# Kernel tuning notes

Hardware: AMD Instinct MI355X
Metric: run time of the kernel (lower is better)

Reference implementation:

```python
import jax, jax.numpy as jnp
import numpy as np

N, E, H, NH, S, EF, K = 25000, 400000, 64, 4, 16, 8, 2
HS = H // NH  # head size


def _ln(x, w, b):
    m = x.mean(-1, keepdims=True)
    v = ((x - m) ** 2).mean(-1, keepdims=True)
    return (x - m) / jnp.sqrt(v + 1e-5) * w + b


def _seg_softmax(scores, seg, n):
    # scores: [E, NH], seg: [E] -> softmax over edges sharing the same dest node
    mx = jax.ops.segment_max(scores, seg, num_segments=n)
    e = jnp.exp(scores - mx[seg])
    s = jax.ops.segment_sum(e, seg, num_segments=n)
    return e / (s[seg] + 1e-9)


def _edge_layer(h, x_s, src, dest, ef, w1, w2, proj, gated):
    # h: [N,H] (already layer-normed). Gather, fused per-edge MLP (no bias).
    inp = jnp.concatenate([h[src], h[dest], x_s[src], x_s[dest], ef], axis=-1)  # [E,168]
    raw = jnp.maximum(inp @ w1.T, 0.0) @ w2.T  # [E,NH]
    if gated:
        w = jax.nn.sigmoid(raw)
    else:
        w = _seg_softmax(jax.nn.leaky_relu(raw) / jnp.sqrt(jnp.asarray(HS, raw.dtype)), dest, N)
    msg = h.reshape(N, NH, HS)[src] * w[:, :, None]          # [E,NH,HS]
    agg = jax.ops.segment_sum(msg, dest, num_segments=N)     # [N,NH,HS]
    return agg.reshape(N, H) @ proj.T, w


def _mlp(x, w1, b1, w2, b2):
    return jnp.maximum(x @ w1.T + b1, 0.0) @ w2.T + b2


def _forward(x, x_s, edge_features, fwd_w1, fwd_w2, fwd_proj, rev_w1, rev_w2, rev_proj,
             ln_w, ln_b, r_w1, r_b1, r_w2, r_b2, z_w1, z_b1, z_w2, z_b2,
             c_w1, c_b1, c_w2, c_b2, edge_index):
    src, dest = edge_index[0], edge_index[1]
    # forward-direction stacked attention hops
    h_fwd, fwd_ws = x, []
    for k in range(K):
        h_norm = _ln(h_fwd, ln_w, ln_b)
        msg, w = _edge_layer(h_norm, x_s, src, dest, edge_features,
                             fwd_w1[k], fwd_w2[k], fwd_proj[k], gated=False)
        h_fwd = h_fwd + msg
        fwd_ws.append(w)
    fwd_ws = jnp.stack(fwd_ws, axis=-1)  # [E,NH,K]
    # reverse-direction stacked gating hops (edge direction flipped)
    h_rev, rev_ws = x, []
    for k in range(K):
        h_norm = _ln(h_rev, ln_w, ln_b)
        msg, w = _edge_layer(h_norm, x_s, dest, src, edge_features,
                             rev_w1[k], rev_w2[k], rev_proj[k], gated=True)
        h_rev = h_rev + msg
        rev_ws.append(w)
    rev_ws = jnp.stack(rev_ws, axis=-1)  # [E,NH,K]
    messages = jnp.concatenate([h_fwd - x, h_rev - x], axis=-1)  # [N,2H]
    gate_input = jnp.concatenate([x, messages], axis=-1)          # [N,3H]
    r_gate = jax.nn.sigmoid(_mlp(gate_input, r_w1, r_b1, r_w2, r_b2))
    z_gate = jax.nn.sigmoid(_mlp(gate_input, z_w1, z_b1, z_w2, z_b2))
    cand_in = jnp.concatenate([r_gate * x, messages], axis=-1)
    cand = jnp.tanh(_mlp(cand_in, c_w1, c_b1, c_w2, c_b2))
    final_h = (1.0 - z_gate) * x + z_gate * cand
    return final_h, fwd_ws, rev_ws, z_gate, r_gate


def setup_inputs() -> dict:
    key = jax.random.key(0)
    ks = jax.random.split(key, 20)
    mlp_in = 2 * H + 2 * S + EF  # 168
    width = 2 * H                # 128
    gi, gw = 3 * H, 3 * H        # 192, 192

    def nrm(k, shape, fan_in):
        return jax.random.normal(k, shape, jnp.float32) / np.sqrt(fan_in)

    return {
        'x': jax.random.normal(ks[0], (N, H), jnp.float32),
        'x_s': jax.random.normal(ks[1], (N, S), jnp.float32),
        'edge_index': jax.random.randint(ks[2], (2, E), 0, N, jnp.int32),
        'edge_features': jax.random.normal(ks[3], (E, EF), jnp.float32),
        'fwd_w1': nrm(ks[4], (K, width, mlp_in), mlp_in),
        'fwd_w2': nrm(ks[5], (K, NH, width), width),
        'fwd_proj': nrm(ks[6], (K, H, H), H),
        'rev_w1': nrm(ks[7], (K, width, mlp_in), mlp_in),
        'rev_w2': nrm(ks[8], (K, NH, width), width),
        'rev_proj': nrm(ks[9], (K, H, H), H),
        'ln_w': jnp.ones((H,), jnp.float32),
        'ln_b': jnp.zeros((H,), jnp.float32),
        'r_w1': nrm(ks[10], (gw, gi), gi), 'r_b1': jnp.zeros((gw,), jnp.float32),
        'r_w2': nrm(ks[11], (H, gw), gw), 'r_b2': jnp.zeros((H,), jnp.float32),
        'z_w1': nrm(ks[12], (gw, gi), gi), 'z_b1': jnp.zeros((gw,), jnp.float32),
        'z_w2': nrm(ks[13], (H, gw), gw), 'z_b2': jnp.zeros((H,), jnp.float32),
        'c_w1': nrm(ks[14], (gw, gi), gi), 'c_b1': jnp.zeros((gw,), jnp.float32),
        'c_w2': nrm(ks[15], (H, gw), gw), 'c_b2': jnp.zeros((H,), jnp.float32),
    }


def reference(x, x_s, edge_index, edge_features, fwd_w1, fwd_w2, fwd_proj,
              rev_w1, rev_w2, rev_proj, ln_w, ln_b, r_w1, r_b1, r_w2, r_b2,
              z_w1, z_b1, z_w2, z_b2, c_w1, c_b1, c_w2, c_b2):
    return _forward(x, x_s, edge_features, fwd_w1, fwd_w2, fwd_proj,
                    rev_w1, rev_w2, rev_proj, ln_w, ln_b,
                    r_w1, r_b1, r_w2, r_b2, z_w1, z_b1, z_w2, z_b2,
                    c_w1, c_b1, c_w2, c_b2, edge_index)
```

## Files before the change

kernel.cpp:

```cpp
#include <hip/hip_runtime.h>
#include <hip/hip_fp16.h>
#include <math.h>

#define NN 25000
#define EE 400000
#define HH 64
#define NHEAD 4
#define SDIM 16
#define EFDIM 8
#define KHOP 2
#define MIN 168
#define WID 128
#define GIN 192
#define KP 96

typedef __attribute__((ext_vector_type(8))) short bf16x8;
typedef __attribute__((ext_vector_type(4))) float f32x4;
typedef unsigned short ushortT;
typedef unsigned int uintT;

__device__ __forceinline__ float wave_sum64(float v) {
#pragma unroll
  for (int m = 1; m <= 32; m <<= 1) v += __shfl_xor(v, m, 64);
  return v;
}

__device__ __forceinline__ ushortT f2b(float f) {
  uintT u = __float_as_uint(f);
  return (ushortT)((u + 0x7FFFu + ((u >> 16) & 1u)) >> 16);
}
__device__ __forceinline__ float b2f(ushortT h) {
  return __uint_as_float(((uintT)h) << 16);
}

union U4H8 {
  uint4 u;
  __half2 h[4];
};

__device__ __forceinline__ __half2 relu2(__half2 v) {
  union { __half2 h; uintT u; } x;
  x.h = v;
  uintT mask = ((x.u & 0x80008000u) >> 15) * 0xFFFFu;
  x.u &= ~mask;
  return x.h;
}

__global__ void k_histo2(const int* __restrict__ src, const int* __restrict__ dst,
                         int* __restrict__ cnt_s, int* __restrict__ cnt_d) {
  int e = blockIdx.x * 256 + threadIdx.x;
  if (e < EE) {
    atomicAdd(&cnt_d[dst[e]], 1);
    atomicAdd(&cnt_s[src[e]], 1);
  }
}

__global__ void k_scan2(const int* __restrict__ cnt_d, const int* __restrict__ cnt_s,
                        int* __restrict__ rp_d, int* __restrict__ rp_s) {
  const int* cnt = blockIdx.x ? cnt_s : cnt_d;
  int* rp = blockIdx.x ? rp_s : rp_d;
  __shared__ int part[1024];
  int t = threadIdx.x;
  const int CH = (NN + 1023) / 1024;
  int base = t * CH;
  int s = 0;
  for (int i = 0; i < CH; ++i) {
    int j = base + i;
    if (j < NN) s += cnt[j];
  }
  part[t] = s;
  __syncthreads();
  for (int off = 1; off < 1024; off <<= 1) {
    int v = (t >= off) ? part[t - off] : 0;
    __syncthreads();
    part[t] += v;
    __syncthreads();
  }
  int run = (t == 0) ? 0 : part[t - 1];
  for (int i = 0; i < CH; ++i) {
    int j = base + i;
    if (j < NN) { rp[j] = run; run += cnt[j]; }
  }
  if (t == 1023) rp[NN] = run;
}

__global__ void k_scatter2(const int* __restrict__ src, const int* __restrict__ dst,
                           const int* __restrict__ rp_s, const int* __restrict__ rp_d,
                           int* __restrict__ cur_s, int* __restrict__ cur_d,
                           int* __restrict__ eid_s, int* __restrict__ eid_d) {
  int e = blockIdx.x * 256 + threadIdx.x;
  if (e < EE) {
    int nd = dst[e];
    int pd = atomicAdd(&cur_d[nd], 1);
    eid_d[rp_d[nd] + pd] = e;
    int ns = src[e];
    int ps = atomicAdd(&cur_s[ns], 1);
    eid_s[rp_s[ns] + ps] = e;
  }
}

__global__ __launch_bounds__(256) void k_sortseg2(const int* __restrict__ rp_d,
                                                  const int* __restrict__ rp_s,
                                                  int* __restrict__ eid_d,
                                                  int* __restrict__ eid_s) {
  int gw = blockIdx.x * 4 + (threadIdx.x >> 6);
  int lane = threadIdx.x & 63;
  if (gw >= 2 * NN) return;
  const int* rp = (gw < NN) ? rp_d : rp_s;
  int* eids = (gw < NN) ? eid_d : eid_s;
  int node = (gw < NN) ? gw : gw - NN;
  int beg = rp[node], end = rp[node + 1];
  int deg = end - beg;
  if (deg <= 1) return;
  if (deg <= 64) {
    int v = (lane < deg) ? eids[beg + lane] : 0x7fffffff;
#pragma unroll
    for (int k = 2; k <= 64; k <<= 1) {
#pragma unroll
      for (int j = k >> 1; j > 0; j >>= 1) {
        int other = __shfl_xor(v, j, 64);
        bool takeMin = (((lane & k) == 0) == ((lane & j) == 0));
        v = takeMin ? min(v, other) : max(v, other);
      }
    }
    if (lane < deg) eids[beg + lane] = v;
  } else if (lane == 0) {
    for (int i = beg + 1; i < end; ++i) {
      int v = eids[i];
      int j = i - 1;
      while (j >= beg && eids[j] > v) { eids[j + 1] = eids[j]; --j; }
      eids[j + 1] = v;
    }
  }
}

__global__ void k_mkpos2(const int* __restrict__ eid_d, const int* __restrict__ eid_s,
                         const int* __restrict__ src, const int* __restrict__ dst,
                         const float* __restrict__ ef, int4* __restrict__ pos_f,
                         int4* __restrict__ pos_r, uint4* __restrict__ efh_f,
                         uint4* __restrict__ efh_r) {
  int i = blockIdx.x * 256 + threadIdx.x;
  if (i >= EE) return;
  int e1 = eid_d[i];
  pos_f[i] = make_int4(e1, src[e1], dst[e1], 0);
  int e2 = eid_s[i];
  pos_r[i] = make_int4(e2, dst[e2], src[e2], 0);
  {
    float4 a0 = *(const float4*)(ef + (size_t)e1 * EFDIM);
    float4 a1 = *(const float4*)(ef + (size_t)e1 * EFDIM + 4);
    U4H8 u;
    u.h[0] = __floats2half2_rn(a0.x, a0.y);
    u.h[1] = __floats2half2_rn(a0.z, a0.w);
    u.h[2] = __floats2half2_rn(a1.x, a1.y);
    u.h[3] = __floats2half2_rn(a1.z, a1.w);
    efh_f[i] = u.u;
  }
  {
    float4 b0 = *(const float4*)(ef + (size_t)e2 * EFDIM);
    float4 b1 = *(const float4*)(ef + (size_t)e2 * EFDIM + 4);
    U4H8 u;
    u.h[0] = __floats2half2_rn(b0.x, b0.y);
    u.h[1] = __floats2half2_rn(b0.z, b0.w);
    u.h[2] = __floats2half2_rn(b1.x, b1.y);
    u.h[3] = __floats2half2_rn(b1.z, b1.w);
    efh_r[i] = u.u;
  }
}

#define PACKN (256 * KP + 512 + 256)
__global__ void k_pack_bf(const float* __restrict__ fw1, const float* __restrict__ rw1,
                          const float* __restrict__ fw2, const float* __restrict__ rw2,
                          ushortT* __restrict__ pAB_all, __half2* __restrict__ w1e2_all,
                          __half2* __restrict__ w22_all) {
  int y = blockIdx.y;
  const float* w1 = (y < 2) ? fw1 + (size_t)y * WID * MIN
                            : rw1 + (size_t)(y - 2) * WID * MIN;
  const float* w2 = (y < 2) ? fw2 + (size_t)y * NHEAD * WID
                            : rw2 + (size_t)(y - 2) * NHEAD * WID;
  int i = blockIdx.x * 256 + threadIdx.x;
  if (i < 256 * KP) {
    int j = i / KP, k = i % KP;
    float v = 0.f;
    if (k < 80) {
      int row = (j < 128) ? j : j - 128;
      int col = (j < 128) ? (k < 64 ? k : k + 64) : (k < 64 ? k + 64 : k + 80);
      v = w1[row * MIN + col];
    }
    pAB_all[(size_t)y * 256 * KP + i] = f2b(v);
  } else if (i < 256 * KP + 512) {
    int jj = i - 256 * KP;
    int f = jj >> 6, jp = jj & 63;
    w1e2_all[y * 512 + jj] =
        __floats2half2_rn(w1[(2 * jp) * MIN + 160 + f], w1[(2 * jp + 1) * MIN + 160 + f]);
  } else if (i < PACKN) {
    int jj = i - 256 * KP - 512;
    int o = jj >> 6, jp = jj & 63;
    w22_all[y * 256 + jj] = __floats2half2_rn(w2[o * WID + 2 * jp], w2[o * WID + 2 * jp + 1]);
  }
}

#define CW1 (GIN * GIN)
#define CW2 (HH * GIN)
__global__ void k_cvt6(const float* __restrict__ r_w1, const float* __restrict__ z_w1,
                       const float* __restrict__ c_w1, const float* __restrict__ r_w2,
                       const float* __restrict__ z_w2, const float* __restrict__ c_w2,
                       ushortT* __restrict__ rzw1, ushortT* __restrict__ cw1,
                       ushortT* __restrict__ rw2, ushortT* __restrict__ zw2,
                       ushortT* __restrict__ cw2) {
  int i = blockIdx.x * 256 + threadIdx.x;
  if (i < CW1) rzw1[i] = f2b(r_w1[i]);
  else if (i < 2 * CW1) rzw1[i] = f2b(z_w1[i - CW1]);
  else if (i < 3 * CW1) cw1[i - 2 * CW1] = f2b(c_w1[i - 2 * CW1]);
  else if (i < 3 * CW1 + CW2) rw2[i - 3 * CW1] = f2b(r_w2[i - 3 * CW1]);
  else if (i < 3 * CW1 + 2 * CW2) zw2[i - 3 * CW1 - CW2] = f2b(z_w2[i - 3 * CW1 - CW2]);
  else if (i < 3 * CW1 + 3 * CW2) cw2[i - 3 * CW1 - 2 * CW2] = f2b(c_w2[i - 3 * CW1 - 2 * CW2]);
}

__global__ __launch_bounds__(256) void k_ln_init(
    const float* __restrict__ x, const float* __restrict__ xs,
    const float* __restrict__ lw, const float* __restrict__ lb,
    ushortT* __restrict__ ncf0, ushortT* __restrict__ ncr0,
    ushortT* __restrict__ ncf1, ushortT* __restrict__ ncr1) {
  int t = threadIdx.x;
  int node = blockIdx.x * 4 + (t >> 6), lane = t & 63;
  if (node >= NN) return;
  float v = x[(size_t)node * HH + lane];
  float mean = wave_sum64(v) * (1.0f / 64.0f);
  float d = v - mean;
  float var = wave_sum64(d * d) * (1.0f / 64.0f);
  ushortT val = f2b(d * rsqrtf(var + 1e-5f) * lw[lane] + lb[lane]);
  ncf0[(size_t)node * KP + lane] = val;
  ncr0[(size_t)node * KP + lane] = val;
  if (lane < SDIM) {
    ushortT xv = f2b(xs[(size_t)node * SDIM + lane]);
    ncf0[(size_t)node * KP + HH + lane] = xv;
    ncr0[(size_t)node * KP + HH + lane] = xv;
    ncf1[(size_t)node * KP + HH + lane] = xv;
    ncr1[(size_t)node * KP + HH + lane] = xv;
    ncf0[(size_t)node * KP + 80 + lane] = 0;
    ncr0[(size_t)node * KP + 80 + lane] = 0;
    ncf1[(size_t)node * KP + 80 + lane] = 0;
    ncr1[(size_t)node * KP + 80 + lane] = 0;
  }
}

__global__ __launch_bounds__(256) void k_proj2(
    const ushortT* __restrict__ Af, const ushortT* __restrict__ Ar,
    const ushortT* __restrict__ Wf, const ushortT* __restrict__ Wr,
    ushortT* __restrict__ Cf, ushortT* __restrict__ Cr) {
  const ushortT* A = blockIdx.y ? Ar : Af;
  const ushortT* W = blockIdx.y ? Wr : Wf;
  ushortT* C = blockIdx.y ? Cr : Cf;
  int w = threadIdx.x >> 6, l = threadIdx.x & 63;
  int m0 = blockIdx.x * 64 + w * 16;
  int rowa = m0 + (l & 15);
  int kb = l >> 4;
  bf16x8 afr0 = {0,0,0,0,0,0,0,0}, afr1 = afr0, afr2 = afr0;
  if (rowa < NN) {
    const ushortT* ap = A + (size_t)rowa * KP + kb * 8;
    afr0 = *(const bf16x8*)(ap);
    afr1 = *(const bf16x8*)(ap + 32);
    afr2 = *(const bf16x8*)(ap + 64);
  }
  int crow = m0 + (l >> 4) * 4;
  int ccol0 = l & 15;
  for (int n0 = 0; n0 < 256; n0 += 64) {
    f32x4 acc[4];
#pragma unroll
    for (int n = 0; n < 4; ++n) acc[n] = (f32x4){0.f, 0.f, 0.f, 0.f};
    const ushortT* wbase = W + (size_t)(n0 + (l & 15)) * KP + kb * 8;
#pragma unroll
    for (int n = 0; n < 4; ++n) {
      const ushortT* wp = wbase + (size_t)(16 * n) * KP;
      acc[n] = __builtin_amdgcn_mfma_f32_16x16x32_bf16(afr0, *(const bf16x8*)(wp), acc[n], 0, 0, 0);
      acc[n] = __builtin_amdgcn_mfma_f32_16x16x32_bf16(afr1, *(const bf16x8*)(wp + 32), acc[n], 0, 0, 0);
      acc[n] = __builtin_amdgcn_mfma_f32_16x16x32_bf16(afr2, *(const bf16x8*)(wp + 64), acc[n], 0, 0, 0);
    }
#pragma unroll
    for (int n = 0; n < 4; ++n) {
      int col = n0 + ccol0 + n * 16;
#pragma unroll
      for (int r = 0; r < 4; ++r) {
        int row = crow + r;
        if (row < NN)
          C[(size_t)row * 256 + col] = __half_as_ushort(__float2half(acc[n][r]));
      }
    }
  }
}

template <int ACT, int BF16OUT, int KD>
__global__ __launch_bounds__(256) void k_gemm2(
    const ushortT* __restrict__ A, int lda, const ushortT* __restrict__ W,
    const float* __restrict__ bias, void* __restrict__ Cout, int ldc, int M, int Nc,
    const float* __restrict__ zv, const float* __restrict__ xp) {
  constexpr int KS = KD / 32;
  int w = threadIdx.x >> 6, l = threadIdx.x & 63;
  int m0 = blockIdx.x * 64 + w * 16;
  int rowa = m0 + (l & 15);
  int kb = l >> 4;
  bf16x8 afr[KS];
#pragma unroll
  for (int ks = 0; ks < KS; ++ks) {
    afr[ks] = (bf16x8){0, 0, 0, 0, 0, 0, 0, 0};
    if (rowa < M) afr[ks] = *(const bf16x8*)(A + (size_t)rowa * lda + ks * 32 + kb * 8);
  }
  int crow = m0 + (l >> 4) * 4;
  int ccol0 = l & 15;
  for (int n0 = 0; n0 < Nc; n0 += 64) {
    f32x4 acc[4];
#pragma unroll
    for (int n = 0; n < 4; ++n) acc[n] = (f32x4){0.f, 0.f, 0.f, 0.f};
    const ushortT* wbase = W + (size_t)(n0 + (l & 15)) * KD + kb * 8;
#pragma unroll
    for (int n = 0; n < 4; ++n) {
      const ushortT* wp = wbase + (size_t)(16 * n) * KD;
#pragma unroll
      for (int ks = 0; ks < KS; ++ks)
        acc[n] = __builtin_amdgcn_mfma_f32_16x16x32_bf16(afr[ks], *(const bf16x8*)(wp + ks * 32),
                                                         acc[n], 0, 0, 0);
    }
#pragma unroll
    for (int n = 0; n < 4; ++n) {
      int col = n0 + ccol0 + n * 16;
      float bv = bias ? bias[col] : 0.f;
#pragma unroll
      for (int r = 0; r < 4; ++r) {
        int row = crow + r;
        if (row < M) {
          float v = acc[n][r] + bv;
          if (ACT == 1) v = fmaxf(v, 0.f);
          else if (ACT == 2) v = 1.f / (1.f + expf(-v));
          else if (ACT == 3) v = tanhf(v);
          else if (ACT == 5) {
            float z = zv[(size_t)row * HH + col];
            float xv = xp[(size_t)row * HH + col];
            v = (1.f - z) * xv + z * tanhf(v);
          }
          if (BF16OUT)
            ((ushortT*)Cout)[(size_t)row * ldc + col] = f2b(v);
          else
            ((float*)Cout)[(size_t)row * ldc + col] = v;
        }
      }
    }
  }
}

__global__ __launch_bounds__(256) void k_gemm_rz(
    const ushortT* __restrict__ hid, const ushortT* __restrict__ rw2,
    const ushortT* __restrict__ zw2, const float* __restrict__ rb2,
    const float* __restrict__ zb2, float* __restrict__ outR, float* __restrict__ outZ,
    const float* __restrict__ x, ushortT* __restrict__ gi) {
  int y = blockIdx.y;
  const ushortT* A = hid + (y ? GIN : 0);
  const ushortT* W = y ? zw2 : rw2;
  const float* bias = y ? zb2 : rb2;
  float* C = y ? outZ : outR;
  constexpr int KS = GIN / 32;
  int w = threadIdx.x >> 6, l = threadIdx.x & 63;
  int m0 = blockIdx.x * 64 + w * 16;
  int rowa = m0 + (l & 15);
  int kb = l >> 4;
  bf16x8 afr[KS];
#pragma unroll
  for (int ks = 0; ks < KS; ++ks) {
    afr[ks] = (bf16x8){0, 0, 0, 0, 0, 0, 0, 0};
    if (rowa < NN) afr[ks] = *(const bf16x8*)(A + (size_t)rowa * 384 + ks * 32 + kb * 8);
  }
  int crow = m0 + (l >> 4) * 4;
  int ccol0 = l & 15;
  f32x4 acc[4];
#pragma unroll
  for (int n = 0; n < 4; ++n) acc[n] = (f32x4){0.f, 0.f, 0.f, 0.f};
  const ushortT* wbase = W + (size_t)(l & 15) * GIN + kb * 8;
#pragma unroll
  for (int n = 0; n < 4; ++n) {
    const ushortT* wp = wbase + (size_t)(16 * n) * GIN;
#pragma unroll
    for (int ks = 0; ks < KS; ++ks)
      acc[n] = __builtin_amdgcn_mfma_f32_16x16x32_bf16(afr[ks], *(const bf16x8*)(wp + ks * 32),
                                                       acc[n], 0, 0, 0);
  }
#pragma unroll
  for (int n = 0; n < 4; ++n) {
    int col = ccol0 + n * 16;
    float bv = bias[col];
#pragma unroll
    for (int r = 0; r < 4; ++r) {
      int row = crow + r;
      if (row < NN) {
        float v = acc[n][r] + bv;
        float sig = 1.f / (1.f + expf(-v));
        C[(size_t)row * HH + col] = sig;
        if (y == 0)
          gi[(size_t)row * GIN + col] = f2b(sig * x[(size_t)row * HH + col]);
      }
    }
  }
}

__global__ __launch_bounds__(256) void k_edge3(
    const ushortT* __restrict__ cABf, const ushortT* __restrict__ cABr,
    const int4* __restrict__ pos_f, const int4* __restrict__ pos_r,
    const uint4* __restrict__ efh_f, const uint4* __restrict__ efh_r,
    const __half2* __restrict__ w1e2_f, const __half2* __restrict__ w1e2_r,
    const __half2* __restrict__ w22_f, const __half2* __restrict__ w22_r,
    float* __restrict__ s_seq, float* __restrict__ outRW,
    float* __restrict__ ws_seq, int hop) {
  int y = blockIdx.y;
  const __half2* cAB2 = (const __half2*)(y ? cABr : cABf);
  const int4* pos = y ? pos_r : pos_f;
  const uint4* efh = y ? efh_r : efh_f;
  const __half2* w1e2 = y ? w1e2_r : w1e2_f;
  const __half2* w22 = y ? w22_r : w22_f;
  __shared__ __half2 w1e2_s[8][64];
  __shared__ __half2 w22_s[4][64];
  int t = threadIdx.x;
  for (int i = t; i < 512; i += 256) w1e2_s[i >> 6][i & 63] = w1e2[i];
  if (t < 256) w22_s[t >> 6][t & 63] = w22[t];
  __syncthreads();
  int es = t >> 2, q = t & 3;
  size_t ii = (size_t)blockIdx.x * 64 + es;
  int4 pr = pos[ii];
  const __half2* cA2 = cAB2 + (size_t)pr.y * 128;
  const __half2* cB2 = cAB2 + (size_t)pr.z * 128 + 64;
  U4H8 efu;
  efu.u = efh[ii];
  __half2 efb[8];
#pragma unroll
  for (int f2v = 0; f2v < 4; ++f2v) {
    efb[2 * f2v] = __half2half2(__low2half(efu.h[f2v]));
    efb[2 * f2v + 1] = __half2half2(__high2half(efu.h[f2v]));
  }
  float pf[4] = {0.f, 0.f, 0.f, 0.f};
#pragma unroll
  for (int c = 0; c < 4; ++c) {
    int jp0 = c * 16 + q * 4;
    U4H8 ua, ub;
    ua.u = *(const uint4*)(cA2 + jp0);
    ub.u = *(const uint4*)(cB2 + jp0);
    __half2 h2v[4];
#pragma unroll
    for (int i2 = 0; i2 < 4; ++i2) h2v[i2] = __hadd2(ua.h[i2], ub.h[i2]);
#pragma unroll
    for (int f = 0; f < 8; ++f) {
      U4H8 wv;
      wv.u = *(const uint4*)(&w1e2_s[f][jp0]);
#pragma unroll
      for (int i2 = 0; i2 < 4; ++i2) h2v[i2] = __hfma2(efb[f], wv.h[i2], h2v[i2]);
    }
#pragma unroll
    for (int i2 = 0; i2 < 4; ++i2) h2v[i2] = relu2(h2v[i2]);
#pragma unroll
    for (int o = 0; o < 4; ++o) {
      U4H8 wv;
      wv.u = *(const uint4*)(&w22_s[o][jp0]);
      __half2 p2 = __hmul2(h2v[0], wv.h[0]);
      p2 = __hfma2(h2v[1], wv.h[1], p2);
      p2 = __hfma2(h2v[2], wv.h[2], p2);
      p2 = __hfma2(h2v[3], wv.h[3], p2);
      pf[o] += __low2float(p2) + __high2float(p2);
    }
  }
#pragma unroll
  for (int m = 1; m <= 2; m <<= 1) {
    pf[0] += __shfl_xor(pf[0], m, 64);
    pf[1] += __shfl_xor(pf[1], m, 64);
    pf[2] += __shfl_xor(pf[2], m, 64);
    pf[3] += __shfl_xor(pf[3], m, 64);
  }
  float pv = (q == 0) ? pf[0] : (q == 1) ? pf[1] : (q == 2) ? pf[2] : pf[3];
  if (y) {
    float sig = 1.f / (1.f + expf(-pv));
    outRW[(size_t)pr.x * (NHEAD * KHOP) + q * KHOP + hop] = sig;
    ws_seq[ii * 4 + q] = sig;
  } else {
    s_seq[ii * 4 + q] = (pv > 0.f ? pv : 0.01f * pv) * 0.25f;
  }
}

template <int DO_LN, int DO_GATE>
__global__ __launch_bounds__(256) void k_softagg4(
    const ushortT* __restrict__ ncf, const ushortT* __restrict__ ncr,
    ushortT* __restrict__ ncf_n, ushortT* __restrict__ ncr_n,
    const float* __restrict__ s_seq, const float* __restrict__ ws_seq, int hop,
    const int* __restrict__ rp_d, const int* __restrict__ rp_s,
    const int4* __restrict__ pos_f, const int4* __restrict__ pos_r,
    const float* __restrict__ proj_f, const float* __restrict__ proj_r,
    float* __restrict__ h_f, float* __restrict__ h_r, float* __restrict__ wout,
    const float* __restrict__ lnw, const float* __restrict__ lnb,
    const float* __restrict__ x, ushortT* __restrict__ gi) {
  int y = blockIdx.y;
  const ushortT* hn_bf = y ? ncr : ncf;
  const int* rp = y ? rp_s : rp_d;
  const int4* pos = y ? pos_r : pos_f;
  const float* proj = y ? proj_r : proj_f;
  float* h = y ? h_r : h_f;
  __shared__ float proj_s[64][68];
  __shared__ float agg_s[4][64];
  __shared__ float w_s[4][64][4];
  __shared__ int ot_s[4][64];
  int t = threadIdx.x;
  for (int i = t; i < 4096; i += 256) proj_s[i >> 6][i & 63] = proj[i];
  int wvi = t >> 6, lane = t & 63;
  __syncthreads();

  for (int it = 0; it < 4; ++it) {
    int node = blockIdx.x * 16 + wvi * 4 + it;
    if (node >= NN) continue;
    int beg = rp[node], end = rp[node + 1];
    int deg = end - beg;
    bool small = (deg <= 64);
    float mxv = 0.f, invv = 0.f;
    int li = lane >> 2, o = lane & 3;
    if (deg > 0 && small) {
      int i0 = beg + li;
      if (y == 0) {
        int ee4[4];
        float sv[4];
#pragma unroll
        for (int u = 0; u < 4; ++u) {
          int idx = i0 + u * 16;
          bool val = idx < end;
          int4 pr = pos[val ? idx : beg];
          ee4[u] = pr.x;
          if (o == 0 && val) ot_s[wvi][li + u * 16] = pr.y * KP;
          float v = s_seq[(size_t)(val ? idx : beg) * 4 + o];
          sv[u] = val ? v : -1e30f;
        }
        float mx = fmaxf(fmaxf(sv[0], sv[1]), fmaxf(sv[2], sv[3]));
#pragma unroll
        for (int m = 4; m <= 32; m <<= 1) mx = fmaxf(mx, __shfl_xor(mx, m, 64));
        float ex[4];
        float sum = 0.f;
#pragma unroll
        for (int u = 0; u < 4; ++u) {
          ex[u] = (sv[u] > -1e29f) ? expf(sv[u] - mx) : 0.f;
          sum += ex[u];
        }
#pragma unroll
        for (int m = 4; m <= 32; m <<= 1) sum += __shfl_xor(sum, m, 64);
        float inv = 1.f / (sum + 1e-9f);
#pragma unroll
        for (int u = 0; u < 4; ++u) {
          if (i0 + u * 16 < end) {
            float wv = ex[u] * inv;
            wout[(size_t)ee4[u] * (NHEAD * KHOP) + o * KHOP + hop] = wv;
            w_s[wvi][li + u * 16][o] = wv;
          }
        }
      } else {
#pragma unroll
        for (int u = 0; u < 4; ++u) {
          int idx = i0 + u * 16;
          bool val = idx < end;
          if (val) {
            if (o == 0) {
              int4 pr = pos[idx];
              ot_s[wvi][li + u * 16] = pr.y * KP;
            }
            w_s[wvi][li + u * 16][o] = ws_seq[(size_t)idx * 4 + o];
          }
        }
      }
    } else if (deg > 0) {
      if (y == 0) {
        float mx = -1e30f;
        for (int ii = beg + li; ii < end; ii += 16)
          mx = fmaxf(mx, s_seq[(size_t)ii * 4 + o]);
#pragma unroll
        for (int m = 4; m <= 32; m <<= 1) mx = fmaxf(mx, __shfl_xor(mx, m, 64));
        float sum = 0.f;
        for (int ii = beg + li; ii < end; ii += 16)
          sum += expf(s_seq[(size_t)ii * 4 + o] - mx);
#pragma unroll
        for (int m = 4; m <= 32; m <<= 1) sum += __shfl_xor(sum, m, 64);
        float inv = 1.f / (sum + 1e-9f);
        for (int ii = beg + li; ii < end; ii += 16) {
          wout[(size_t)pos[ii].x * (NHEAD * KHOP) + o * KHOP + hop] =
              expf(s_seq[(size_t)ii * 4 + o] - mx) * inv;
        }
        mxv = mx;
        invv = inv;
      }
    }
    int hd = lane >> 4;
    float acc = 0.f;
    if (small) {
      for (int ii = 0; ii < deg; ii += 8) {
#pragma unroll
        for (int u = 0; u < 8; ++u) {
          int ed = ii + u;
          int edc = (ed < deg) ? ed : 0;
          int ot = ot_s[wvi][edc];
          float w = w_s[wvi][edc][hd];
          float hv = b2f(hn_bf[(size_t)ot + lane]);
          acc += ((ed < deg) ? w : 0.f) * hv;
        }
      }
    } else {
      float mx_hd = 0.f, inv_hd = 0.f;
      if (y == 0) {
        mx_hd = __shfl(mxv, hd, 64);
        inv_hd = __shfl(invv, hd, 64);
      }
      for (int ii = beg; ii < end; ++ii) {
        int4 pr = pos[ii];
        float w;
        if (y == 0)
          w = expf(s_seq[(size_t)ii * 4 + hd] - mx_hd) * inv_hd;
        else
          w = ws_seq[(size_t)ii * 4 + hd];
        acc += w * b2f(hn_bf[(size_t)pr.y * KP + lane]);
      }
    }
    agg_s[wvi][lane] = acc;
    float m = 0.f;
#pragma unroll
    for (int hh = 0; hh < 64; hh += 4) {
      float4 p = *(const float4*)(&proj_s[lane][hh]);
      m += p.x * agg_s[wvi][hh] + p.y * agg_s[wvi][hh + 1] +
           p.z * agg_s[wvi][hh + 2] + p.w * agg_s[wvi][hh + 3];
    }
    size_t g = (size_t)node * HH + lane;
    float hnew = h[g] + m;
    h[g] = hnew;
    if (DO_LN) {
      float mean = wave_sum64(hnew) * (1.0f / 64.0f);
      float d = hnew - mean;
      float var = wave_sum64(d * d) * (1.0f / 64.0f);
      ushortT val = f2b(d * rsqrtf(var + 1e-5f) * lnw[lane] + lnb[lane]);
      (y ? ncr_n : ncf_n)[(size_t)node * KP + lane] = val;
    }
    if (DO_GATE) {
      float xv = x[g];
      if (y == 0) {
        gi[(size_t)node * GIN + lane] = f2b(xv);
        gi[(size_t)node * GIN + 64 + lane] = f2b(hnew - xv);
      } else {
        gi[(size_t)node * GIN + 128 + lane] = f2b(hnew - xv);
      }
    }
  }
}

extern "C" void kernel_launch(void* const* d_in, const int* in_sizes, int n_in,
                              void* d_out, int out_size, void* d_ws, size_t ws_size,
                              hipStream_t stream) {
  const float* x = (const float*)d_in[0];
  const float* xs = (const float*)d_in[1];
  const int* ei = (const int*)d_in[2];
  const float* ef = (const float*)d_in[3];
  const float* fw1 = (const float*)d_in[4];
  const float* fw2 = (const float*)d_in[5];
  const float* fpj = (const float*)d_in[6];
  const float* rw1 = (const float*)d_in[7];
  const float* rw2 = (const float*)d_in[8];
  const float* rpj = (const float*)d_in[9];
  const float* lnw = (const float*)d_in[10];
  const float* lnb = (const float*)d_in[11];
  const float* r_w1 = (const float*)d_in[12];
  const float* r_b1 = (const float*)d_in[13];
  const float* r_w2 = (const float*)d_in[14];
  const float* r_b2 = (const float*)d_in[15];
  const float* z_w1 = (const float*)d_in[16];
  const float* z_b1 = (const float*)d_in[17];
  const float* z_w2 = (const float*)d_in[18];
  const float* z_b2 = (const float*)d_in[19];
  const float* c_w1 = (const float*)d_in[20];
  const float* c_b1 = (const float*)d_in[21];
  const float* c_w2 = (const float*)d_in[22];
  const float* c_b2 = (const float*)d_in[23];
  const int* srcp = ei;
  const int* dstp = ei + EE;

  float* outF = (float*)d_out;
  float* outFW = outF + (size_t)NN * HH;
  float* outRW = outFW + (size_t)EE * NHEAD * KHOP;
  float* outZ = outRW + (size_t)EE * NHEAD * KHOP;
  float* outR = outZ + (size_t)NN * HH;

  char* Wb = (char*)d_ws;
  size_t off = 0;
  auto alloc = [&](size_t bytes) -> void* {
    void* p = Wb + off;
    off += (bytes + 255) & ~(size_t)255;
    return p;
  };
  float* h_fwd = (float*)alloc((size_t)NN * HH * 4);
  float* h_rev = (float*)alloc((size_t)NN * HH * 4);
  ushortT* ncat_f0 = (ushortT*)alloc((size_t)NN * KP * 2);
  ushortT* ncat_r0 = (ushortT*)alloc((size_t)NN * KP * 2);
  ushortT* ncat_f1 = (ushortT*)alloc((size_t)NN * KP * 2);
  ushortT* ncat_r1 = (ushortT*)alloc((size_t)NN * KP * 2);
  float* s_seq = (float*)alloc((size_t)EE * NHEAD * 4);
  float* ws_seq = (float*)alloc((size_t)EE * NHEAD * 4);
  char* big = (char*)alloc((size_t)2 * NN * 256 * 2);
  ushortT* cAB_f = (ushortT*)big;
  ushortT* cAB_r = (ushortT*)(big + (size_t)NN * 256 * 2);
  ushortT* hid_bf = (ushortT*)big;
  ushortT* gi_bf = (ushortT*)alloc((size_t)NN * GIN * 2);
  ushortT* packAB_bf = (ushortT*)alloc((size_t)4 * 256 * KP * 2);
  __half2* w1e2h = (__half2*)alloc((size_t)4 * 512 * 4);
  __half2* w22h = (__half2*)alloc((size_t)4 * 256 * 4);
  ushortT* rzw1_bf = (ushortT*)alloc((size_t)384 * GIN * 2);
  ushortT* rw2_bf = (ushortT*)alloc((size_t)HH * GIN * 2);
  ushortT* zw2_bf = (ushortT*)alloc((size_t)HH * GIN * 2);
  ushortT* cw1_bf = (ushortT*)alloc((size_t)GIN * GIN * 2);
  ushortT* cw2_bf = (ushortT*)alloc((size_t)HH * GIN * 2);
  float* rz_b1 = (float*)alloc(384 * 4);
  int* rp_d = (int*)alloc((NN + 8) * 4);
  int* rp_s = (int*)alloc((NN + 8) * 4);
  int* cur2 = (int*)alloc((size_t)2 * NN * 4);
  int* cur_d = cur2;
  int* cur_s = cur2 + NN;
  int* eid_d = (int*)alloc((size_t)EE * 4);
  int* eid_s = (int*)alloc((size_t)EE * 4);
  int4* pos_f = (int4*)alloc((size_t)EE * 16);
  int4* pos_r = (int4*)alloc((size_t)EE * 16);
  uint4* efh_f = (uint4*)alloc((size_t)EE * 16);
  uint4* efh_r = (uint4*)alloc((size_t)EE * 16);

  (void)hipMemcpyAsync(h_fwd, x, (size_t)NN * HH * 4, hipMemcpyDeviceToDevice, stream);
  (void)hipMemcpyAsync(h_rev, x, (size_t)NN * HH * 4, hipMemcpyDeviceToDevice, stream);
  (void)hipMemcpyAsync(rz_b1, r_b1, GIN * 4, hipMemcpyDeviceToDevice, stream);
  (void)hipMemcpyAsync(rz_b1 + GIN, z_b1, GIN * 4, hipMemcpyDeviceToDevice, stream);

  const int EB = (EE + 255) / 256, NW = (NN + 3) / 4;
  const int PB = (PACKN + 255) / 256;

  dim3 gPack(PB, 4);
  k_pack_bf<<<gPack, 256, 0, stream>>>(fw1, rw1, fw2, rw2, packAB_bf, w1e2h, w22h);
  k_cvt6<<<(3 * CW1 + 3 * CW2 + 255) / 256, 256, 0, stream>>>(
      r_w1, z_w1, c_w1, r_w2, z_w2, c_w2, rzw1_bf, cw1_bf, rw2_bf, zw2_bf, cw2_bf);

  (void)hipMemsetAsync(cur2, 0, (size_t)2 * NN * 4, stream);
  k_histo2<<<EB, 256, 0, stream>>>(srcp, dstp, cur_s, cur_d);
  k_scan2<<<2, 1024, 0, stream>>>(cur_d, cur_s, rp_d, rp_s);
  (void)hipMemsetAsync(cur2, 0, (size_t)2 * NN * 4, stream);
  k_scatter2<<<EB, 256, 0, stream>>>(srcp, dstp, rp_s, rp_d, cur_s, cur_d, eid_s, eid_d);
  k_sortseg2<<<(2 * NN + 3) / 4, 256, 0, stream>>>(rp_d, rp_s, eid_d, eid_s);
  k_mkpos2<<<EB, 256, 0, stream>>>(eid_d, eid_s, srcp, dstp, ef, pos_f, pos_r, efh_f, efh_r);

  k_ln_init<<<NW, 256, 0, stream>>>(x, xs, lnw, lnb, ncat_f0, ncat_r0, ncat_f1, ncat_r1);

  const int MB64 = (NN + 63) / 64;
  const int NB16 = (NN + 15) / 16;
  dim3 gProj(MB64, 2), gEdge(EE / 64, 2), gAgg(NB16, 2);
  for (int k = 0; k < KHOP; ++k) {
    const ushortT* nf = k ? ncat_f1 : ncat_f0;
    const ushortT* nr = k ? ncat_r1 : ncat_r0;
    k_proj2<<<gProj, 256, 0, stream>>>(nf, nr,
                                       packAB_bf + (size_t)k * 256 * KP,
                                       packAB_bf + (size_t)(2 + k) * 256 * KP,
                                       cAB_f, cAB_r);
    k_edge3<<<gEdge, 256, 0, stream>>>(cAB_f, cAB_r, pos_f, pos_r, efh_f, efh_r,
                                       w1e2h + (size_t)k * 512,
                                       w1e2h + (size_t)(2 + k) * 512,
                                       w22h + (size_t)k * 256,
                                       w22h + (size_t)(2 + k) * 256,
                                       s_seq, outRW, ws_seq, k);
    if (k == 0)
      k_softagg4<1, 0><<<gAgg, 256, 0, stream>>>(
          nf, nr, ncat_f1, ncat_r1, s_seq, ws_seq, k, rp_d, rp_s, pos_f, pos_r,
          fpj + (size_t)k * HH * HH, rpj + (size_t)k * HH * HH, h_fwd, h_rev, outFW,
          lnw, lnb, x, gi_bf);
    else
      k_softagg4<0, 1><<<gAgg, 256, 0, stream>>>(
          nf, nr, ncat_f1, ncat_r1, s_seq, ws_seq, k, rp_d, rp_s, pos_f, pos_r,
          fpj + (size_t)k * HH * HH, rpj + (size_t)k * HH * HH, h_fwd, h_rev, outFW,
          lnw, lnb, x, gi_bf);
  }

  k_gemm2<1, 1, GIN><<<MB64, 256, 0, stream>>>(gi_bf, GIN, rzw1_bf, rz_b1, hid_bf,
                                               384, NN, 384, nullptr, nullptr);
  dim3 gRZ(MB64, 2);
  k_gemm_rz<<<gRZ, 256, 0, stream>>>(hid_bf, rw2_bf, zw2_bf, r_b2, z_b2, outR, outZ,
                                     x, gi_bf);
  k_gemm2<1, 1, GIN><<<MB64, 256, 0, stream>>>(gi_bf, GIN, cw1_bf, c_b1, hid_bf, GIN,
                                               NN, GIN, nullptr, nullptr);
  k_gemm2<5, 0, GIN><<<MB64, 256, 0, stream>>>(hid_bf, GIN, cw2_bf, c_b2, outF, HH,
                                               NN, HH, outZ, x);
}
```

Measured before the change: 533.9 us.

## Split aggregation from projection and run projection plus LayerNorm on MFMA

The fused softmax-aggregate kernel used to also apply the 64x64 projection per node with scalar FMAs from shared memory, then the residual and LayerNorm. This splits it into an aggregation kernel (one node per wave, writing bf16 aggregates) and a separate kernel that does the projection with bf16 MFMA, followed by the residual, LayerNorm and gate-input writes. Projection weights are converted to bf16 in the packing kernel. In exchange it adds an extra kernel launch per hop, a bf16 round-trip of the aggregates through global memory, and lower precision in the projection.

```diff
diff --git a/kernel.cpp b/kernel.cpp
--- a/kernel.cpp
+++ b/kernel.cpp
@@ -167,16 +167,19 @@
   }
 }
 
-#define PACKN (256 * KP + 512 + 256)
+#define PACKN (256 * KP + 512 + 256 + 4096)
 __global__ void k_pack_bf(const float* __restrict__ fw1, const float* __restrict__ rw1,
                           const float* __restrict__ fw2, const float* __restrict__ rw2,
+                          const float* __restrict__ fpj, const float* __restrict__ rpj,
                           ushortT* __restrict__ pAB_all, __half2* __restrict__ w1e2_all,
-                          __half2* __restrict__ w22_all) {
+                          __half2* __restrict__ w22_all, ushortT* __restrict__ pj_all) {
   int y = blockIdx.y;
   const float* w1 = (y < 2) ? fw1 + (size_t)y * WID * MIN
                             : rw1 + (size_t)(y - 2) * WID * MIN;
   const float* w2 = (y < 2) ? fw2 + (size_t)y * NHEAD * WID
                             : rw2 + (size_t)(y - 2) * NHEAD * WID;
+  const float* pj = (y < 2) ? fpj + (size_t)y * HH * HH
+                            : rpj + (size_t)(y - 2) * HH * HH;
   int i = blockIdx.x * 256 + threadIdx.x;
   if (i < 256 * KP) {
     int j = i / KP, k = i % KP;
@@ -192,10 +195,13 @@
     int f = jj >> 6, jp = jj & 63;
     w1e2_all[y * 512 + jj] =
         __floats2half2_rn(w1[(2 * jp) * MIN + 160 + f], w1[(2 * jp + 1) * MIN + 160 + f]);
-  } else if (i < PACKN) {
+  } else if (i < 256 * KP + 512 + 256) {
     int jj = i - 256 * KP - 512;
     int o = jj >> 6, jp = jj & 63;
     w22_all[y * 256 + jj] = __floats2half2_rn(w2[o * WID + 2 * jp], w2[o * WID + 2 * jp + 1]);
+  } else if (i < PACKN) {
+    int jj = i - 256 * KP - 512 - 256;
+    pj_all[y * 4096 + jj] = f2b(pj[jj]);
   }
 }
 
@@ -480,166 +486,203 @@
   }
 }
 
-template <int DO_LN, int DO_GATE>
-__global__ __launch_bounds__(256) void k_softagg4(
+__global__ __launch_bounds__(256) void k_softagg5(
     const ushortT* __restrict__ ncf, const ushortT* __restrict__ ncr,
-    ushortT* __restrict__ ncf_n, ushortT* __restrict__ ncr_n,
     const float* __restrict__ s_seq, const float* __restrict__ ws_seq, int hop,
     const int* __restrict__ rp_d, const int* __restrict__ rp_s,
     const int4* __restrict__ pos_f, const int4* __restrict__ pos_r,
-    const float* __restrict__ proj_f, const float* __restrict__ proj_r,
-    float* __restrict__ h_f, float* __restrict__ h_r, float* __restrict__ wout,
-    const float* __restrict__ lnw, const float* __restrict__ lnb,
-    const float* __restrict__ x, ushortT* __restrict__ gi) {
+    ushortT* __restrict__ agg_f, ushortT* __restrict__ agg_r,
+    float* __restrict__ wout) {
   int y = blockIdx.y;
   const ushortT* hn_bf = y ? ncr : ncf;
   const int* rp = y ? rp_s : rp_d;
   const int4* pos = y ? pos_r : pos_f;
-  const float* proj = y ? proj_r : proj_f;
-  float* h = y ? h_r : h_f;
-  __shared__ float proj_s[64][68];
-  __shared__ float agg_s[4][64];
+  ushortT* agg = y ? agg_r : agg_f;
   __shared__ float w_s[4][64][4];
   __shared__ int ot_s[4][64];
   int t = threadIdx.x;
-  for (int i = t; i < 4096; i += 256) proj_s[i >> 6][i & 63] = proj[i];
   int wvi = t >> 6, lane = t & 63;
-  __syncthreads();
-
-  for (int it = 0; it < 4; ++it) {
-    int node = blockIdx.x * 16 + wvi * 4 + it;
-    if (node >= NN) continue;
-    int beg = rp[node], end = rp[node + 1];
-    int deg = end - beg;
-    bool small = (deg <= 64);
-    float mxv = 0.f, invv = 0.f;
-    int li = lane >> 2, o = lane & 3;
-    if (deg > 0 && small) {
-      int i0 = beg + li;
-      if (y == 0) {
-        int ee4[4];
-        float sv[4];
-#pragma unroll
-        for (int u = 0; u < 4; ++u) {
-          int idx = i0 + u * 16;
-          bool val = idx < end;
-          int4 pr = pos[val ? idx : beg];
-          ee4[u] = pr.x;
-          if (o == 0 && val) ot_s[wvi][li + u * 16] = pr.y * KP;
-          float v = s_seq[(size_t)(val ? idx : beg) * 4 + o];
-          sv[u] = val ? v : -1e30f;
+  int node = blockIdx.x * 4 + wvi;
+  if (node >= NN) return;
+  int beg = rp[node], end = rp[node + 1];
+  int deg = end - beg;
+  bool small = (deg <= 64);
+  float mxv = 0.f, invv = 0.f;
+  int li = lane >> 2, o = lane & 3;
+  if (deg > 0 && small) {
+    int i0 = beg + li;
+    if (y == 0) {
+      int ee4[4];
+      float sv[4];
+#pragma unroll
+      for (int u = 0; u < 4; ++u) {
+        int idx = i0 + u * 16;
+        bool val = idx < end;
+        int4 pr = pos[val ? idx : beg];
+        ee4[u] = pr.x;
+        if (o == 0 && val) ot_s[wvi][li + u * 16] = pr.y * KP;
+        float v = s_seq[(size_t)(val ? idx : beg) * 4 + o];
+        sv[u] = val ? v : -1e30f;
+      }
+      float mx = fmaxf(fmaxf(sv[0], sv[1]), fmaxf(sv[2], sv[3]));
+#pragma unroll
+      for (int m = 4; m <= 32; m <<= 1) mx = fmaxf(mx, __shfl_xor(mx, m, 64));
+      float ex[4];
+      float sum = 0.f;
+#pragma unroll
+      for (int u = 0; u < 4; ++u) {
+        ex[u] = (sv[u] > -1e29f) ? expf(sv[u] - mx) : 0.f;
+        sum += ex[u];
+      }
+#pragma unroll
+      for (int m = 4; m <= 32; m <<= 1) sum += __shfl_xor(sum, m, 64);
+      float inv = 1.f / (sum + 1e-9f);
+#pragma unroll
+      for (int u = 0; u < 4; ++u) {
+        if (i0 + u * 16 < end) {
+          float wv = ex[u] * inv;
+          wout[(size_t)ee4[u] * (NHEAD * KHOP) + o * KHOP + hop] = wv;
+          w_s[wvi][li + u * 16][o] = wv;
         }
-        float mx = fmaxf(fmaxf(sv[0], sv[1]), fmaxf(sv[2], sv[3]));
-#pragma unroll
-        for (int m = 4; m <= 32; m <<= 1) mx = fmaxf(mx, __shfl_xor(mx, m, 64));
-        float ex[4];
-        float sum = 0.f;
-#pragma unroll
-        for (int u = 0; u < 4; ++u) {
-          ex[u] = (sv[u] > -1e29f) ? expf(sv[u] - mx) : 0.f;
-          sum += ex[u];
+      }
+    } else {
+#pragma unroll
+      for (int u = 0; u < 4; ++u) {
+        int idx = i0 + u * 16;
+        bool val = idx < end;
+        if (val) {
+          if (o == 0) {
+            int4 pr = pos[idx];
+            ot_s[wvi][li + u * 16] = pr.y * KP;
+          }
+          w_s[wvi][li + u * 16][o] = ws_seq[(size_t)idx * 4 + o];
         }
-#pragma unroll
-        for (int m = 4; m <= 32; m <<= 1) sum += __shfl_xor(sum, m, 64);
-        float inv = 1.f / (sum + 1e-9f);
-#pragma unroll
-        for (int u = 0; u < 4; ++u) {
-          if (i0 + u * 16 < end) {
-            float wv = ex[u] * inv;
-            wout[(size_t)ee4[u] * (NHEAD * KHOP) + o * KHOP + hop] = wv;
-            w_s[wvi][li + u * 16][o] = wv;
-          }
+      }
+    }
+  } else if (deg > 0) {
+    if (y == 0) {
+      float mx = -1e30f;
+      for (int ii = beg + li; ii < end; ii += 16)
+        mx = fmaxf(mx, s_seq[(size_t)ii * 4 + o]);
+#pragma unroll
+      for (int m = 4; m <= 32; m <<= 1) mx = fmaxf(mx, __shfl_xor(mx, m, 64));
+      float sum = 0.f;
+      for (int ii = beg + li; ii < end; ii += 16)
+        sum += expf(s_seq[(size_t)ii * 4 + o] - mx);
+#pragma unroll
+      for (int m = 4; m <= 32; m <<= 1) sum += __shfl_xor(sum, m, 64);
+      float inv = 1.f / (sum + 1e-9f);
+      for (int ii = beg + li; ii < end; ii += 16) {
+        wout[(size_t)pos[ii].x * (NHEAD * KHOP) + o * KHOP + hop] =
+            expf(s_seq[(size_t)ii * 4 + o] - mx) * inv;
+      }
+      mxv = mx;
+      invv = inv;
+    }
+  }
+  int hd = lane >> 4;
+  float acc = 0.f;
+  if (small) {
+    for (int ii = 0; ii < deg; ii += 8) {
+#pragma unroll
+      for (int u = 0; u < 8; ++u) {
+        int ed = ii + u;
+        int edc = (ed < deg) ? ed : 0;
+        int ot = ot_s[wvi][edc];
+        float w = w_s[wvi][edc][hd];
+        float hv = b2f(hn_bf[(size_t)ot + lane]);
+        acc += ((ed < deg) ? w : 0.f) * hv;
+      }
+    }
+  } else {
+    float mx_hd = 0.f, inv_hd = 0.f;
+    if (y == 0) {
+      mx_hd = __shfl(mxv, hd, 64);
+      inv_hd = __shfl(invv, hd, 64);
+    }
+    for (int ii = beg; ii < end; ++ii) {
+      int4 pr = pos[ii];
+      float w;
+      if (y == 0)
+        w = expf(s_seq[(size_t)ii * 4 + hd] - mx_hd) * inv_hd;
+      else
+        w = ws_seq[(size_t)ii * 4 + hd];
+      acc += w * b2f(hn_bf[(size_t)pr.y * KP + lane]);
+    }
+  }
+  agg[(size_t)node * HH + lane] = f2b(acc);
+}
+
+template <int DO_LN, int DO_GATE>
+__global__ __launch_bounds__(256) void k_projout(
+    const ushortT* __restrict__ agg_f, const ushortT* __restrict__ agg_r,
+    const ushortT* __restrict__ pj_f, const ushortT* __restrict__ pj_r,
+    float* __restrict__ h_f, float* __restrict__ h_r,
+    ushortT* __restrict__ ncf_n, ushortT* __restrict__ ncr_n,
+    const float* __restrict__ lnw, const float* __restrict__ lnb,
+    const float* __restrict__ x, ushortT* __restrict__ gi) {
+  int y = blockIdx.y;
+  const ushortT* A = y ? agg_r : agg_f;
+  const ushortT* W = y ? pj_r : pj_f;
+  float* h = y ? h_r : h_f;
+  ushortT* ncat_n = y ? ncr_n : ncf_n;
+  int w = threadIdx.x >> 6, l = threadIdx.x & 63;
+  int m0 = blockIdx.x * 64 + w * 16;
+  int rowa = m0 + (l & 15);
+  int kb = l >> 4;
+  bf16x8 afr0 = {0, 0, 0, 0, 0, 0, 0, 0}, afr1 = afr0;
+  if (rowa < NN) {
+    afr0 = *(const bf16x8*)(A + (size_t)rowa * HH + kb * 8);
+    afr1 = *(const bf16x8*)(A + (size_t)rowa * HH + 32 + kb * 8);
+  }
+  f32x4 acc[4];
+#pragma unroll
+  for (int n = 0; n < 4; ++n) acc[n] = (f32x4){0.f, 0.f, 0.f, 0.f};
+  const ushortT* wbase = W + (size_t)(l & 15) * HH + kb * 8;
+#pragma unroll
+  for (int n = 0; n < 4; ++n) {
+    const ushortT* wp = wbase + (size_t)(16 * n) * HH;
+    acc[n] = __builtin_amdgcn_mfma_f32_16x16x32_bf16(afr0, *(const bf16x8*)(wp), acc[n], 0, 0, 0);
+    acc[n] = __builtin_amdgcn_mfma_f32_16x16x32_bf16(afr1, *(const bf16x8*)(wp + 32), acc[n], 0, 0, 0);
+  }
+  int crow = m0 + (l >> 4) * 4;
+  int ccol0 = l & 15;
+#pragma unroll
+  for (int r = 0; r < 4; ++r) {
+    int row = crow + r;
+    if (row >= NN) continue;
+    float hv[4];
+#pragma unroll
+    for (int n = 0; n < 4; ++n)
+      hv[n] = h[(size_t)row * HH + ccol0 + n * 16] + acc[n][r];
+    float s = hv[0] + hv[1] + hv[2] + hv[3];
+#pragma unroll
+    for (int m = 1; m <= 8; m <<= 1) s += __shfl_xor(s, m, 64);
+    float mean = s * (1.0f / 64.0f);
+    float ss = 0.f;
+#pragma unroll
+    for (int n = 0; n < 4; ++n) {
+      float d = hv[n] - mean;
+      ss += d * d;
+    }
+#pragma unroll
+    for (int m = 1; m <= 8; m <<= 1) ss += __shfl_xor(ss, m, 64);
+    float rstd = rsqrtf(ss * (1.0f / 64.0f) + 1e-5f);
+#pragma unroll
+    for (int n = 0; n < 4; ++n) {
+      int col = ccol0 + n * 16;
+      size_t g = (size_t)row * HH + col;
+      h[g] = hv[n];
+      if (DO_LN)
+        ncat_n[(size_t)row * KP + col] = f2b((hv[n] - mean) * rstd * lnw[col] + lnb[col]);
+      if (DO_GATE) {
+        float xv = x[g];
+        if (y == 0) {
+          gi[(size_t)row * GIN + col] = f2b(xv);
+          gi[(size_t)row * GIN + 64 + col] = f2b(hv[n] - xv);
+        } else {
+          gi[(size_t)row * GIN + 128 + col] = f2b(hv[n] - xv);
         }
-      } else {
-#pragma unroll
-        for (int u = 0; u < 4; ++u) {
-          int idx = i0 + u * 16;
-          bool val = idx < end;
-          if (val) {
-            if (o == 0) {
-              int4 pr = pos[idx];
-              ot_s[wvi][li + u * 16] = pr.y * KP;
-            }
-            w_s[wvi][li + u * 16][o] = ws_seq[(size_t)idx * 4 + o];
-          }
-        }
-      }
-    } else if (deg > 0) {
-      if (y == 0) {
-        float mx = -1e30f;
-        for (int ii = beg + li; ii < end; ii += 16)
-          mx = fmaxf(mx, s_seq[(size_t)ii * 4 + o]);
-#pragma unroll
-        for (int m = 4; m <= 32; m <<= 1) mx = fmaxf(mx, __shfl_xor(mx, m, 64));
-        float sum = 0.f;
-        for (int ii = beg + li; ii < end; ii += 16)
-          sum += expf(s_seq[(size_t)ii * 4 + o] - mx);
-#pragma unroll
-        for (int m = 4; m <= 32; m <<= 1) sum += __shfl_xor(sum, m, 64);
-        float inv = 1.f / (sum + 1e-9f);
-        for (int ii = beg + li; ii < end; ii += 16) {
-          wout[(size_t)pos[ii].x * (NHEAD * KHOP) + o * KHOP + hop] =
-              expf(s_seq[(size_t)ii * 4 + o] - mx) * inv;
-        }
-        mxv = mx;
-        invv = inv;
-      }
-    }
-    int hd = lane >> 4;
-    float acc = 0.f;
-    if (small) {
-      for (int ii = 0; ii < deg; ii += 8) {
-#pragma unroll
-        for (int u = 0; u < 8; ++u) {
-          int ed = ii + u;
-          int edc = (ed < deg) ? ed : 0;
-          int ot = ot_s[wvi][edc];
-          float w = w_s[wvi][edc][hd];
-          float hv = b2f(hn_bf[(size_t)ot + lane]);
-          acc += ((ed < deg) ? w : 0.f) * hv;
-        }
-      }
-    } else {
-      float mx_hd = 0.f, inv_hd = 0.f;
-      if (y == 0) {
-        mx_hd = __shfl(mxv, hd, 64);
-        inv_hd = __shfl(invv, hd, 64);
-      }
-      for (int ii = beg; ii < end; ++ii) {
-        int4 pr = pos[ii];
-        float w;
-        if (y == 0)
-          w = expf(s_seq[(size_t)ii * 4 + hd] - mx_hd) * inv_hd;
-        else
-          w = ws_seq[(size_t)ii * 4 + hd];
-        acc += w * b2f(hn_bf[(size_t)pr.y * KP + lane]);
-      }
-    }
-    agg_s[wvi][lane] = acc;
-    float m = 0.f;
-#pragma unroll
-    for (int hh = 0; hh < 64; hh += 4) {
-      float4 p = *(const float4*)(&proj_s[lane][hh]);
-      m += p.x * agg_s[wvi][hh] + p.y * agg_s[wvi][hh + 1] +
-           p.z * agg_s[wvi][hh + 2] + p.w * agg_s[wvi][hh + 3];
-    }
-    size_t g = (size_t)node * HH + lane;
-    float hnew = h[g] + m;
-    h[g] = hnew;
-    if (DO_LN) {
-      float mean = wave_sum64(hnew) * (1.0f / 64.0f);
-      float d = hnew - mean;
-      float var = wave_sum64(d * d) * (1.0f / 64.0f);
-      ushortT val = f2b(d * rsqrtf(var + 1e-5f) * lnw[lane] + lnb[lane]);
-      (y ? ncr_n : ncf_n)[(size_t)node * KP + lane] = val;
-    }
-    if (DO_GATE) {
-      float xv = x[g];
-      if (y == 0) {
-        gi[(size_t)node * GIN + lane] = f2b(xv);
-        gi[(size_t)node * GIN + 64 + lane] = f2b(hnew - xv);
-      } else {
-        gi[(size_t)node * GIN + 128 + lane] = f2b(hnew - xv);
       }
     }
   }
@@ -701,9 +744,12 @@
   ushortT* cAB_r = (ushortT*)(big + (size_t)NN * 256 * 2);
   ushortT* hid_bf = (ushortT*)big;
   ushortT* gi_bf = (ushortT*)alloc((size_t)NN * GIN * 2);
+  ushortT* agg_f = (ushortT*)alloc((size_t)NN * HH * 2);
+  ushortT* agg_r = (ushortT*)alloc((size_t)NN * HH * 2);
   ushortT* packAB_bf = (ushortT*)alloc((size_t)4 * 256 * KP * 2);
   __half2* w1e2h = (__half2*)alloc((size_t)4 * 512 * 4);
   __half2* w22h = (__half2*)alloc((size_t)4 * 256 * 4);
+  ushortT* pj_bf = (ushortT*)alloc((size_t)4 * 4096 * 2);
   ushortT* rzw1_bf = (ushortT*)alloc((size_t)384 * GIN * 2);
   ushortT* rw2_bf = (ushortT*)alloc((size_t)HH * GIN * 2);
   ushortT* zw2_bf = (ushortT*)alloc((size_t)HH * GIN * 2);
@@ -731,7 +777,8 @@
   const int PB = (PACKN + 255) / 256;
 
   dim3 gPack(PB, 4);
-  k_pack_bf<<<gPack, 256, 0, stream>>>(fw1, rw1, fw2, rw2, packAB_bf, w1e2h, w22h);
+  k_pack_bf<<<gPack, 256, 0, stream>>>(fw1, rw1, fw2, rw2, fpj, rpj, packAB_bf,
+                                       w1e2h, w22h, pj_bf);
   k_cvt6<<<(3 * CW1 + 3 * CW2 + 255) / 256, 256, 0, stream>>>(
       r_w1, z_w1, c_w1, r_w2, z_w2, c_w2, rzw1_bf, cw1_bf, rw2_bf, zw2_bf, cw2_bf);
 
@@ -746,8 +793,7 @@
   k_ln_init<<<NW, 256, 0, stream>>>(x, xs, lnw, lnb, ncat_f0, ncat_r0, ncat_f1, ncat_r1);
 
   const int MB64 = (NN + 63) / 64;
-  const int NB16 = (NN + 15) / 16;
-  dim3 gProj(MB64, 2), gEdge(EE / 64, 2), gAgg(NB16, 2);
+  dim3 gProj(MB64, 2), gEdge(EE / 64, 2), gAgg(NW, 2), gPO(MB64, 2);
   for (int k = 0; k < KHOP; ++k) {
     const ushortT* nf = k ? ncat_f1 : ncat_f0;
     const ushortT* nr = k ? ncat_r1 : ncat_r0;
@@ -761,16 +807,16 @@
                                        w22h + (size_t)k * 256,
                                        w22h + (size_t)(2 + k) * 256,
                                        s_seq, outRW, ws_seq, k);
+    k_softagg5<<<gAgg, 256, 0, stream>>>(nf, nr, s_seq, ws_seq, k, rp_d, rp_s,
+                                         pos_f, pos_r, agg_f, agg_r, outFW);
     if (k == 0)
-      k_softagg4<1, 0><<<gAgg, 256, 0, stream>>>(
-          nf, nr, ncat_f1, ncat_r1, s_seq, ws_seq, k, rp_d, rp_s, pos_f, pos_r,
-          fpj + (size_t)k * HH * HH, rpj + (size_t)k * HH * HH, h_fwd, h_rev, outFW,
-          lnw, lnb, x, gi_bf);
+      k_projout<1, 0><<<gPO, 256, 0, stream>>>(
+          agg_f, agg_r, pj_bf + (size_t)k * 4096, pj_bf + (size_t)(2 + k) * 4096,
+          h_fwd, h_rev, ncat_f1, ncat_r1, lnw, lnb, x, gi_bf);
     else
-      k_softagg4<0, 1><<<gAgg, 256, 0, stream>>>(
-          nf, nr, ncat_f1, ncat_r1, s_seq, ws_seq, k, rp_d, rp_s, pos_f, pos_r,
-          fpj + (size_t)k * HH * HH, rpj + (size_t)k * HH * HH, h_fwd, h_rev, outFW,
-          lnw, lnb, x, gi_bf);
+      k_projout<0, 1><<<gPO, 256, 0, stream>>>(
+          agg_f, agg_r, pj_bf + (size_t)k * 4096, pj_bf + (size_t)(2 + k) * 4096,
+          h_fwd, h_rev, ncat_f1, ncat_r1, lnw, lnb, x, gi_bf);
   }
 
   k_gemm2<1, 1, GIN><<<MB64, 256, 0, stream>>>(gi_bf, GIN, rzw1_bf, rz_b1, hid_bf,
```

New measurement: 517.6 us. 1.03x faster.
